# Kernel optimization log

Hardware: AMD Instinct MI355X
Metric: run time of the kernel (lower is better)

## Reference

```python
import jax, jax.numpy as jnp
import numpy as np

N_NODES = 100000
N_EDGES = 1600000
D_IN = 64
HID = 128
N_LAYERS = 5
N_GRAPHS = 128
D_OUT = 10


def setup_inputs() -> dict:
    key = jax.random.key(0)
    ks = jax.random.split(key, 12)
    x = jax.random.normal(ks[0], (N_NODES, D_IN), dtype=jnp.float32)
    edge_index = jax.random.randint(ks[1], (2, N_EDGES), 0, N_NODES, dtype=jnp.int64)
    batch = jnp.sort(jax.random.randint(ks[2], (N_NODES,), 0, N_GRAPHS, dtype=jnp.int64))
    s = 0.05
    W_emb = jax.random.normal(ks[3], (D_IN, HID), dtype=jnp.float32) * s
    b_emb = jnp.zeros((HID,), dtype=jnp.float32)
    W_conv = jax.random.normal(ks[4], (N_LAYERS, HID, HID), dtype=jnp.float32) * s
    b_conv = jnp.zeros((N_LAYERS, HID), dtype=jnp.float32)
    W1 = jax.random.normal(ks[5], (3 * HID, 3 * HID // 2), dtype=jnp.float32) * s
    b1 = jnp.zeros((3 * HID // 2,), dtype=jnp.float32)
    W2 = jax.random.normal(ks[6], (3 * HID // 2, D_OUT), dtype=jnp.float32) * s
    b2 = jnp.zeros((D_OUT,), dtype=jnp.float32)
    return {"x": x, "edge_index": edge_index, "batch": batch,
            "W_emb": W_emb, "b_emb": b_emb, "W_conv": W_conv, "b_conv": b_conv,
            "W1": W1, "b1": b1, "W2": W2, "b2": b2}


def _forward(x, edge_index, batch, W_emb, b_emb, W_conv, b_conv, W1, b1, W2, b2):
    N = x.shape[0]
    # input embedding
    h = x @ W_emb + b_emb
    # GCN normalization with self-loops (PyG GCNConv default)
    self_idx = jnp.arange(N, dtype=edge_index.dtype)
    src = jnp.concatenate([edge_index[0], self_idx])
    dst = jnp.concatenate([edge_index[1], self_idx])
    deg = jax.ops.segment_sum(jnp.ones_like(dst, dtype=h.dtype), dst, num_segments=N)
    dinv = jnp.where(deg > 0, jax.lax.rsqrt(jnp.maximum(deg, 1e-12)), 0.0)
    norm = dinv[src] * dinv[dst]  # [E+N]
    for l in range(N_LAYERS):
        hw = h @ W_conv[l]
        msg = hw[src] * norm[:, None]              # [E+N, HID] gather
        agg = jax.ops.segment_sum(msg, dst, num_segments=N)  # scatter-add
        h = jnp.tanh(agg + b_conv[l])
    # global add / max / mean pooling over graphs
    sum_p = jax.ops.segment_sum(h, batch, num_segments=N_GRAPHS)
    cnt = jax.ops.segment_sum(jnp.ones((N,), dtype=h.dtype), batch, num_segments=N_GRAPHS)
    mean_p = sum_p / jnp.maximum(cnt, 1.0)[:, None]
    max_p = jax.ops.segment_max(h, batch, num_segments=N_GRAPHS)
    max_p = jnp.where(jnp.isfinite(max_p), max_p, 0.0)
    g = jnp.concatenate([sum_p, max_p, mean_p], axis=1)  # [G, 3*HID]
    g = jax.nn.leaky_relu(g @ W1 + b1, negative_slope=0.01)
    g = jax.nn.leaky_relu(g @ W2 + b2, negative_slope=0.01)
    return g


def reference(x, edge_index, batch, W_emb, b_emb, W_conv, b_conv, W1, b1, W2, b2):
    return _forward(x, edge_index, batch, W_emb, b_emb, W_conv, b_conv, W1, b1, W2, b2)
```

## Files before the change

### kernel.cpp

```cpp
#include <hip/hip_runtime.h>
#include <hip/hip_fp16.h>
#include <math.h>

typedef _Float16 f16x4 __attribute__((ext_vector_type(4)));
typedef float    f32x4 __attribute__((ext_vector_type(4)));

template<int K>
__global__ void convert_w_k(const float* __restrict__ W, __half* __restrict__ Wt,
                            int total)
{
    int i = blockIdx.x * 256 + threadIdx.x;
    if (i >= total) return;
    const int nk = 128 * K;
    const int l = i / nk;
    const int rem = i % nk;
    const int n = rem / K;
    const int k = rem % K;
    Wt[i] = __float2half(W[(size_t)l * nk + k * 128 + n]);
}

template<int K, bool HAS_BIAS, bool OUT_HALF>
__global__ __launch_bounds__(256) void dense_mfma_k(
    const float* __restrict__ A, const __half* __restrict__ Wt,
    const float* __restrict__ bias, const float* __restrict__ rowscale,
    void* __restrict__ out_, int M)
{
    constexpr int KP = K + 8;
    __shared__ _Float16 Ah[64 * KP];
    __shared__ _Float16 Wl[128 * KP];

    const int t = threadIdx.x;
    const long row0 = (long)blockIdx.x * 64;

    constexpr int KQ8 = K / 8;
    constexpr int KQ4 = K / 4;

    for (int i = t; i < K * 16; i += 256) {
        const int n = i / KQ8;
        const int kq = i % KQ8;
        *(float4*)&Wl[n * KP + kq * 8] = *(const float4*)&Wt[n * K + kq * 8];
    }
    for (int i = t; i < K * 16; i += 256) {
        const int r = i / KQ4;
        const int kq = i % KQ4;
        long gr = row0 + r; if (gr > (long)M - 1) gr = (long)M - 1;
        const float4 v = *(const float4*)&A[gr * K + kq * 4];
        f16x4 h4 = { (_Float16)v.x, (_Float16)v.y, (_Float16)v.z, (_Float16)v.w };
        *(f16x4*)&Ah[r * KP + kq * 4] = h4;
    }
    __syncthreads();

    const int wid = t >> 6;
    const int lane = t & 63;
    const int lrow = lane & 15;
    const int lk = (lane >> 4) * 4;

    f32x4 acc[8];
#pragma unroll
    for (int c = 0; c < 8; c++) acc[c] = f32x4{0.f, 0.f, 0.f, 0.f};

#pragma unroll
    for (int kc = 0; kc < K / 16; kc++) {
        const int kbase = kc * 16 + lk;
        const f16x4 a = *(const f16x4*)&Ah[(wid * 16 + lrow) * KP + kbase];
#pragma unroll
        for (int c = 0; c < 8; c++) {
            const f16x4 b = *(const f16x4*)&Wl[(c * 16 + lrow) * KP + kbase];
            acc[c] = __builtin_amdgcn_mfma_f32_16x16x16f16(a, b, acc[c], 0, 0, 0);
        }
    }

    const int orow = wid * 16 + (lane >> 4) * 4;
#pragma unroll
    for (int r = 0; r < 4; r++) {
        const long grow = row0 + orow + r;
        if (grow < M) {
            if constexpr (OUT_HALF) {
                const float sc = rowscale[grow];
#pragma unroll
                for (int c = 0; c < 8; c++)
                    ((__half*)out_)[grow * 128 + c * 16 + lrow] =
                        __float2half(acc[c][r] * sc);
            } else {
#pragma unroll
                for (int c = 0; c < 8; c++) {
                    float v = acc[c][r];
                    if (HAS_BIAS) v += bias[c * 16 + lrow];
                    ((float*)out_)[grow * 128 + c * 16 + lrow] = v;
                }
            }
        }
    }
}

__global__ void count_edges_k(const int* __restrict__ dst, int* __restrict__ cnt,
                              int* __restrict__ rank, int E)
{
    int e = blockIdx.x * 256 + threadIdx.x;
    if (e < E) rank[e] = atomicAdd(&cnt[dst[e]], 1);
}

__global__ void dinv_k(const int* __restrict__ cnt, float* __restrict__ dinv, int N)
{
    int i = blockIdx.x * 256 + threadIdx.x;
    if (i < N) dinv[i] = rsqrtf((float)cnt[i] + 1.0f);
}

__global__ void scan_block_k(const int* __restrict__ cnt, int* __restrict__ offs,
                             int* __restrict__ bsums, int N)
{
    __shared__ int tmp[256];
    int i = blockIdx.x * 256 + threadIdx.x;
    int v = (i < N) ? cnt[i] : 0;
    tmp[threadIdx.x] = v;
    __syncthreads();
    for (int off = 1; off < 256; off <<= 1) {
        int add = (threadIdx.x >= off) ? tmp[threadIdx.x - off] : 0;
        __syncthreads();
        tmp[threadIdx.x] += add;
        __syncthreads();
    }
    if (i < N) offs[i] = tmp[threadIdx.x] - v;
    if (threadIdx.x == 255) bsums[blockIdx.x] = tmp[255];
}

__global__ void scan_tops_k(int* __restrict__ bsums, int nb)
{
    __shared__ int tmp[512];
    int t = threadIdx.x;
    int v = (t < nb) ? bsums[t] : 0;
    tmp[t] = v;
    __syncthreads();
    for (int off = 1; off < 512; off <<= 1) {
        int add = (t >= off) ? tmp[t - off] : 0;
        __syncthreads();
        tmp[t] += add;
        __syncthreads();
    }
    if (t < nb) bsums[t] = tmp[t] - v;
}

__global__ void scan_add_k(int* __restrict__ offs, const int* __restrict__ bsums,
                           int N, int E)
{
    int i = blockIdx.x * 256 + threadIdx.x;
    if (i < N) offs[i] += bsums[blockIdx.x];
    if (i == 0) offs[N] = E;
}

__global__ void fill_csr_k(const int* __restrict__ src, const int* __restrict__ dst,
                           const int* __restrict__ offs, const int* __restrict__ rank,
                           int* __restrict__ csr, int E)
{
    int e = blockIdx.x * 256 + threadIdx.x;
    if (e >= E) return;
    csr[offs[dst[e]] + rank[e]] = src[e];
}

__global__ __launch_bounds__(256) void aggregate_k(
    const __half2* __restrict__ hws2, const int* __restrict__ offs,
    const int* __restrict__ csr, const float* __restrict__ dinv,
    const float* __restrict__ bconv, float* __restrict__ hout, int N)
{
    const int wid = threadIdx.x >> 6;
    const int lane = threadIdx.x & 63;
    const int half = lane >> 5;
    const int l32 = lane & 31;
    const long node = (long)blockIdx.x * 4 + wid;
    if (node >= N) return;

    float4 acc = make_float4(0.f, 0.f, 0.f, 0.f);

    if (half == 0) {
        const uint2 v = *(const uint2*)&hws2[node * 64 + l32 * 2];
        const float2 a = __half22float2(__builtin_bit_cast(__half2, v.x));
        const float2 b = __half22float2(__builtin_bit_cast(__half2, v.y));
        acc.x = a.x; acc.y = a.y; acc.z = b.x; acc.w = b.y;
    }

    int k = offs[node];
    const int end = offs[node + 1];

    while (k + 8 <= end) {
        int s[4];
#pragma unroll
        for (int j = 0; j < 4; j++) s[j] = csr[k + 2 * j + half];
        uint2 v[4];
#pragma unroll
        for (int j = 0; j < 4; j++)
            v[j] = *(const uint2*)&hws2[(long)s[j] * 64 + l32 * 2];
#pragma unroll
        for (int j = 0; j < 4; j++) {
            const float2 a = __half22float2(__builtin_bit_cast(__half2, v[j].x));
            const float2 b = __half22float2(__builtin_bit_cast(__half2, v[j].y));
            acc.x += a.x; acc.y += a.y; acc.z += b.x; acc.w += b.y;
        }
        k += 8;
    }
    while (k + 2 <= end) {
        const int s = csr[k + half];
        const uint2 v = *(const uint2*)&hws2[(long)s * 64 + l32 * 2];
        const float2 a = __half22float2(__builtin_bit_cast(__half2, v.x));
        const float2 b = __half22float2(__builtin_bit_cast(__half2, v.y));
        acc.x += a.x; acc.y += a.y; acc.z += b.x; acc.w += b.y;
        k += 2;
    }
    if (k < end && half == 0) {
        const int s = csr[k];
        const uint2 v = *(const uint2*)&hws2[(long)s * 64 + l32 * 2];
        const float2 a = __half22float2(__builtin_bit_cast(__half2, v.x));
        const float2 b = __half22float2(__builtin_bit_cast(__half2, v.y));
        acc.x += a.x; acc.y += a.y; acc.z += b.x; acc.w += b.y;
    }

    acc.x += __shfl_xor(acc.x, 32);
    acc.y += __shfl_xor(acc.y, 32);
    acc.z += __shfl_xor(acc.z, 32);
    acc.w += __shfl_xor(acc.w, 32);

    if (half == 0) {
        const float di = dinv[node];
        const float4 b = *(const float4*)&bconv[l32 * 4];
        float4 o;
        o.x = tanhf(acc.x * di + b.x);
        o.y = tanhf(acc.y * di + b.y);
        o.z = tanhf(acc.z * di + b.z);
        o.w = tanhf(acc.w * di + b.w);
        *(float4*)&hout[node * 128 + l32 * 4] = o;
    }
}

__global__ void graph_bounds_k(const int* __restrict__ batch, int* __restrict__ goffs,
                               int N, int G)
{
    int i = blockIdx.x * 256 + threadIdx.x;
    if (i >= N) return;
    int b = batch[i];
    int prev = (i == 0) ? -1 : batch[i - 1];
    for (int g = prev + 1; g <= b; g++) goffs[g] = i;
    if (i == N - 1)
        for (int g = b + 1; g <= G; g++) goffs[g] = N;
}

__device__ __forceinline__ unsigned enc_f32(float x)
{
    unsigned u = __float_as_uint(x);
    return (u & 0x80000000u) ? ~u : (u | 0x80000000u);
}
__device__ __forceinline__ float dec_f32(unsigned u)
{
    return (u & 0x80000000u) ? __uint_as_float(u ^ 0x80000000u)
                             : __uint_as_float(~u);
}

#define POOL_CHUNK 32

__global__ __launch_bounds__(128) void pool_partial_k(
    const float* __restrict__ h, const int* __restrict__ batch,
    float* __restrict__ sums, unsigned* __restrict__ maxu, int N)
{
    const int t = threadIdx.x;
    const int lane = t & 31;
    const int sub = t >> 5;
    const int f4 = lane * 4;
    const int i0 = blockIdx.x * POOL_CHUNK;
    const int i1 = min(i0 + POOL_CHUNK, N);

    int cur = -1;
    float4 s = make_float4(0.f, 0.f, 0.f, 0.f);
    float4 m = make_float4(-INFINITY, -INFINITY, -INFINITY, -INFINITY);

#pragma unroll 4
    for (int i = i0 + sub; i < i1; i += 4) {
        const int b = batch[i];
        const float4 v = *(const float4*)&h[(long)i * 128 + f4];
        if (b != cur) {
            if (cur >= 0) {
                atomicAdd(&sums[cur * 128 + f4 + 0], s.x);
                atomicAdd(&sums[cur * 128 + f4 + 1], s.y);
                atomicAdd(&sums[cur * 128 + f4 + 2], s.z);
                atomicAdd(&sums[cur * 128 + f4 + 3], s.w);
                atomicMax(&maxu[cur * 128 + f4 + 0], enc_f32(m.x));
                atomicMax(&maxu[cur * 128 + f4 + 1], enc_f32(m.y));
                atomicMax(&maxu[cur * 128 + f4 + 2], enc_f32(m.z));
                atomicMax(&maxu[cur * 128 + f4 + 3], enc_f32(m.w));
            }
            s = make_float4(0.f, 0.f, 0.f, 0.f);
            m = make_float4(-INFINITY, -INFINITY, -INFINITY, -INFINITY);
            cur = b;
        }
        s.x += v.x; s.y += v.y; s.z += v.z; s.w += v.w;
        m.x = fmaxf(m.x, v.x); m.y = fmaxf(m.y, v.y);
        m.z = fmaxf(m.z, v.z); m.w = fmaxf(m.w, v.w);
    }
    if (cur >= 0) {
        atomicAdd(&sums[cur * 128 + f4 + 0], s.x);
        atomicAdd(&sums[cur * 128 + f4 + 1], s.y);
        atomicAdd(&sums[cur * 128 + f4 + 2], s.z);
        atomicAdd(&sums[cur * 128 + f4 + 3], s.w);
        atomicMax(&maxu[cur * 128 + f4 + 0], enc_f32(m.x));
        atomicMax(&maxu[cur * 128 + f4 + 1], enc_f32(m.y));
        atomicMax(&maxu[cur * 128 + f4 + 2], enc_f32(m.z));
        atomicMax(&maxu[cur * 128 + f4 + 3], enc_f32(m.w));
    }
}

__global__ __launch_bounds__(128) void pool_final_k(
    const float* __restrict__ sums, const unsigned* __restrict__ maxu,
    const int* __restrict__ goffs, float* __restrict__ gout)
{
    const int g = blockIdx.x, f = threadIdx.x;
    const int cnt = goffs[g + 1] - goffs[g];
    const float s = sums[g * 128 + f];
    float mx = (cnt > 0) ? dec_f32(maxu[g * 128 + f]) : 0.0f;
    if (!isfinite(mx)) mx = 0.0f;
    const float mean = s / fmaxf((float)cnt, 1.0f);
    gout[g * 384 + f]       = s;
    gout[g * 384 + 128 + f] = mx;
    gout[g * 384 + 256 + f] = mean;
}

__global__ __launch_bounds__(192) void mlp_k(const float* __restrict__ gbuf,
                                             const float* __restrict__ W1,
                                             const float* __restrict__ b1,
                                             const float* __restrict__ W2,
                                             const float* __restrict__ b2,
                                             float* __restrict__ out)
{
    __shared__ float gr[384];
    __shared__ float g1[192];
    const int g = blockIdx.x, t = threadIdx.x;
    for (int i = t; i < 384; i += 192) gr[i] = gbuf[g * 384 + i];
    __syncthreads();
    float acc = b1[t];
    for (int k = 0; k < 384; k++) acc += gr[k] * W1[k * 192 + t];
    acc = acc > 0.f ? acc : 0.01f * acc;
    g1[t] = acc;
    __syncthreads();
    if (t < 10) {
        float a = b2[t];
        for (int k = 0; k < 192; k++) a += g1[k] * W2[k * 10 + t];
        a = a > 0.f ? a : 0.01f * a;
        out[g * 10 + t] = a;
    }
}

extern "C" void kernel_launch(void* const* d_in, const int* in_sizes, int n_in,
                              void* d_out, int out_size, void* d_ws, size_t ws_size,
                              hipStream_t stream)
{
    const float* x      = (const float*)d_in[0];
    const int*   ei     = (const int*)d_in[1];
    const int*   batch  = (const int*)d_in[2];
    const float* W_emb  = (const float*)d_in[3];
    const float* b_emb  = (const float*)d_in[4];
    const float* W_conv = (const float*)d_in[5];
    const float* b_conv = (const float*)d_in[6];
    const float* W1     = (const float*)d_in[7];
    const float* b1     = (const float*)d_in[8];
    const float* W2     = (const float*)d_in[9];
    const float* b2     = (const float*)d_in[10];
    float* out = (float*)d_out;

    const int N  = in_sizes[2];
    const int E  = in_sizes[1] / 2;
    const int G  = 128;
    const int NL = 5;
    const int HID = 128;

    const int* e_src = ei;
    const int* e_dst = ei + E;

    char* ws = (char*)d_ws;
    size_t off = 0;
    auto alloc = [&](size_t bytes) -> void* {
        void* p = ws + off;
        off += (bytes + 255) & ~(size_t)255;
        return p;
    };
    float*    hbuf     = (float*)   alloc((size_t)N * HID * 4);
    __half*   hwbuf    = (__half*)  alloc((size_t)N * HID * 2);
    __half*   wt16     = (__half*)  alloc((size_t)NL * HID * HID * 2);
    __half*   wt16e    = (__half*)  alloc((size_t)64 * HID * 2);
    float*    dinv     = (float*)   alloc((size_t)N * 4);
    int*      cnt      = (int*)     alloc((size_t)N * 4);
    int*      offs     = (int*)     alloc((size_t)(N + 1) * 4);
    int*      bsums    = (int*)     alloc(512 * 4);
    int*      csr      = (int*)     alloc((size_t)E * 4);
    int*      rank     = (int*)     alloc((size_t)E * 4);
    int*      goffs    = (int*)     alloc((size_t)(G + 1) * 4);
    float*    gbuf     = (float*)   alloc((size_t)G * 384 * 4);
    float*    psums    = (float*)   alloc((size_t)G * 128 * 4);
    unsigned* pmaxu    = (unsigned*)alloc((size_t)G * 128 * 4);

    const int nb_nodes = (N + 255) / 256;
    const int nb_edges = (E + 255) / 256;

    const int wtot = NL * HID * HID;
    convert_w_k<128><<<(wtot + 255) / 256, 256, 0, stream>>>(W_conv, wt16, wtot);
    convert_w_k<64><<<(64 * HID + 255) / 256, 256, 0, stream>>>(W_emb, wt16e,
                                                                64 * HID);

    (void)hipMemsetAsync(cnt, 0, (size_t)N * 4, stream);
    count_edges_k<<<nb_edges, 256, 0, stream>>>(e_dst, cnt, rank, E);
    dinv_k<<<nb_nodes, 256, 0, stream>>>(cnt, dinv, N);

    scan_block_k<<<nb_nodes, 256, 0, stream>>>(cnt, offs, bsums, N);
    scan_tops_k<<<1, 512, 0, stream>>>(bsums, nb_nodes);
    scan_add_k<<<nb_nodes, 256, 0, stream>>>(offs, bsums, N, E);

    fill_csr_k<<<nb_edges, 256, 0, stream>>>(e_src, e_dst, offs, rank, csr, E);

    dense_mfma_k<64, true, false><<<(N + 63) / 64, 256, 0, stream>>>(
        x, wt16e, b_emb, nullptr, hbuf, N);

    for (int l = 0; l < NL; l++) {
        dense_mfma_k<128, false, true><<<(N + 63) / 64, 256, 0, stream>>>(
            hbuf, wt16 + (size_t)l * HID * HID, nullptr, dinv, hwbuf, N);
        aggregate_k<<<(N + 3) / 4, 256, 0, stream>>>(
            (const __half2*)hwbuf, offs, csr, dinv,
            b_conv + (size_t)l * HID, hbuf, N);
    }

    graph_bounds_k<<<nb_nodes, 256, 0, stream>>>(batch, goffs, N, G);
    (void)hipMemsetAsync(psums, 0, (size_t)G * 128 * 4, stream);
    (void)hipMemsetAsync(pmaxu, 0, (size_t)G * 128 * 4, stream);
    pool_partial_k<<<(N + POOL_CHUNK - 1) / POOL_CHUNK, 128, 0, stream>>>(
        hbuf, batch, psums, pmaxu, N);
    pool_final_k<<<G, 128, 0, stream>>>(psums, pmaxu, goffs, gbuf);

    mlp_k<<<G, 192, 0, stream>>>(gbuf, W1, b1, W2, b2, out);
}
```

Measured before the change: 698.4 us.

## Fuse GCN aggregation with next layer's dense transform via shared-memory tile

Adds a kernel that aggregates neighbor features for 64 nodes per block, applies dinv scaling, bias and tanh, stores the result as fp16 in shared memory, then multiplies by the next layer's weights with MFMA and writes the scaled fp16 output. This removes the fp32 hbuf write and re-read between the aggregate and dense kernels for the inner layers and halves the kernel launches. The cost is ping-pong buffers and lower gather parallelism per block (4 waves covering 64 nodes serially). It also rounds intermediate activations to fp16 before the matmul.

```diff
diff --git a/kernel.cpp b/kernel.cpp
--- a/kernel.cpp
+++ b/kernel.cpp
@@ -89,6 +89,119 @@
                     ((float*)out_)[grow * 128 + c * 16 + lrow] = v;
                 }
             }
+        }
+    }
+}
+
+__global__ __launch_bounds__(256) void agg_dense_k(
+    const __half2* __restrict__ hws2, const int* __restrict__ offs,
+    const int* __restrict__ csr, const float* __restrict__ dinv,
+    const float* __restrict__ bconv, const __half* __restrict__ Wt,
+    __half* __restrict__ outws, int N)
+{
+    constexpr int KP = 136;
+    __shared__ _Float16 Ah[64 * KP];
+
+    const int t = threadIdx.x;
+    const int wid = t >> 6;
+    const int lane = t & 63;
+    const int half = lane >> 5;
+    const int l32 = lane & 31;
+    const long row0 = (long)blockIdx.x * 64;
+
+    for (int sub = 0; sub < 16; sub++) {
+        const int lr = sub * 4 + wid;
+        const long node = row0 + lr;
+
+        if (node < N) {
+            float4 acc = make_float4(0.f, 0.f, 0.f, 0.f);
+            if (half == 0) {
+                const uint2 v = *(const uint2*)&hws2[node * 64 + l32 * 2];
+                const float2 a = __half22float2(__builtin_bit_cast(__half2, v.x));
+                const float2 b = __half22float2(__builtin_bit_cast(__half2, v.y));
+                acc.x = a.x; acc.y = a.y; acc.z = b.x; acc.w = b.y;
+            }
+            int k = offs[node];
+            const int end = offs[node + 1];
+            while (k + 8 <= end) {
+                int s[4];
+#pragma unroll
+                for (int j = 0; j < 4; j++) s[j] = csr[k + 2 * j + half];
+                uint2 v[4];
+#pragma unroll
+                for (int j = 0; j < 4; j++)
+                    v[j] = *(const uint2*)&hws2[(long)s[j] * 64 + l32 * 2];
+#pragma unroll
+                for (int j = 0; j < 4; j++) {
+                    const float2 a = __half22float2(__builtin_bit_cast(__half2, v[j].x));
+                    const float2 b = __half22float2(__builtin_bit_cast(__half2, v[j].y));
+                    acc.x += a.x; acc.y += a.y; acc.z += b.x; acc.w += b.y;
+                }
+                k += 8;
+            }
+            while (k + 2 <= end) {
+                const int s = csr[k + half];
+                const uint2 v = *(const uint2*)&hws2[(long)s * 64 + l32 * 2];
+                const float2 a = __half22float2(__builtin_bit_cast(__half2, v.x));
+                const float2 b = __half22float2(__builtin_bit_cast(__half2, v.y));
+                acc.x += a.x; acc.y += a.y; acc.z += b.x; acc.w += b.y;
+                k += 2;
+            }
+            if (k < end && half == 0) {
+                const int s = csr[k];
+                const uint2 v = *(const uint2*)&hws2[(long)s * 64 + l32 * 2];
+                const float2 a = __half22float2(__builtin_bit_cast(__half2, v.x));
+                const float2 b = __half22float2(__builtin_bit_cast(__half2, v.y));
+                acc.x += a.x; acc.y += a.y; acc.z += b.x; acc.w += b.y;
+            }
+            acc.x += __shfl_xor(acc.x, 32);
+            acc.y += __shfl_xor(acc.y, 32);
+            acc.z += __shfl_xor(acc.z, 32);
+            acc.w += __shfl_xor(acc.w, 32);
+
+            if (half == 0) {
+                const float di = dinv[node];
+                const float4 b = *(const float4*)&bconv[l32 * 4];
+                f16x4 h4;
+                h4[0] = (_Float16)tanhf(acc.x * di + b.x);
+                h4[1] = (_Float16)tanhf(acc.y * di + b.y);
+                h4[2] = (_Float16)tanhf(acc.z * di + b.z);
+                h4[3] = (_Float16)tanhf(acc.w * di + b.w);
+                *(f16x4*)&Ah[lr * KP + l32 * 4] = h4;
+            }
+        } else if (half == 0) {
+            *(f16x4*)&Ah[lr * KP + l32 * 4] = f16x4{0, 0, 0, 0};
+        }
+    }
+    __syncthreads();
+
+    const int lrow = lane & 15;
+    const int lk = (lane >> 4) * 4;
+
+    f32x4 acc[8];
+#pragma unroll
+    for (int c = 0; c < 8; c++) acc[c] = f32x4{0.f, 0.f, 0.f, 0.f};
+
+#pragma unroll
+    for (int kc = 0; kc < 8; kc++) {
+        const int kbase = kc * 16 + lk;
+        const f16x4 a = *(const f16x4*)&Ah[(wid * 16 + lrow) * KP + kbase];
+#pragma unroll
+        for (int c = 0; c < 8; c++) {
+            const f16x4 b = *(const f16x4*)&Wt[(c * 16 + lrow) * 128 + kbase];
+            acc[c] = __builtin_amdgcn_mfma_f32_16x16x16f16(a, b, acc[c], 0, 0, 0);
+        }
+    }
+
+    const int orow = wid * 16 + (lane >> 4) * 4;
+#pragma unroll
+    for (int r = 0; r < 4; r++) {
+        const long grow = row0 + orow + r;
+        if (grow < N) {
+            const float sc = dinv[grow];
+#pragma unroll
+            for (int c = 0; c < 8; c++)
+                outws[grow * 128 + c * 16 + lrow] = __float2half(acc[c][r] * sc);
         }
     }
 }
@@ -379,7 +492,8 @@
         return p;
     };
     float*    hbuf     = (float*)   alloc((size_t)N * HID * 4);
-    __half*   hwbuf    = (__half*)  alloc((size_t)N * HID * 2);
+    __half*   hwA      = (__half*)  alloc((size_t)N * HID * 2);
+    __half*   hwB      = (__half*)  alloc((size_t)N * HID * 2);
     __half*   wt16     = (__half*)  alloc((size_t)NL * HID * HID * 2);
     __half*   wt16e    = (__half*)  alloc((size_t)64 * HID * 2);
     float*    dinv     = (float*)   alloc((size_t)N * 4);
@@ -414,13 +528,22 @@
     dense_mfma_k<64, true, false><<<(N + 63) / 64, 256, 0, stream>>>(
         x, wt16e, b_emb, nullptr, hbuf, N);
 
-    for (int l = 0; l < NL; l++) {
-        dense_mfma_k<128, false, true><<<(N + 63) / 64, 256, 0, stream>>>(
-            hbuf, wt16 + (size_t)l * HID * HID, nullptr, dinv, hwbuf, N);
-        aggregate_k<<<(N + 3) / 4, 256, 0, stream>>>(
-            (const __half2*)hwbuf, offs, csr, dinv,
-            b_conv + (size_t)l * HID, hbuf, N);
-    }
+    dense_mfma_k<128, false, true><<<(N + 63) / 64, 256, 0, stream>>>(
+        hbuf, wt16, nullptr, dinv, hwA, N);
+
+    __half* cur = hwA;
+    __half* nxt = hwB;
+    for (int l = 0; l < NL - 1; l++) {
+        agg_dense_k<<<(N + 63) / 64, 256, 0, stream>>>(
+            (const __half2*)cur, offs, csr, dinv,
+            b_conv + (size_t)l * HID,
+            wt16 + (size_t)(l + 1) * HID * HID, nxt, N);
+        __half* tmp = cur; cur = nxt; nxt = tmp;
+    }
+
+    aggregate_k<<<(N + 3) / 4, 256, 0, stream>>>(
+        (const __half2*)cur, offs, csr, dinv,
+        b_conv + (size_t)(NL - 1) * HID, hbuf, N);
 
     graph_bounds_k<<<nb_nodes, 256, 0, stream>>>(batch, goffs, N, G);
     (void)hipMemsetAsync(psums, 0, (size_t)G * 128 * 4, stream);
```

New measurement: 1.008 ms. +44.3%, slower.
